# Optimization experiments

Hardware: AMD Instinct MI355X
Metric: run time of the kernel (lower is better)

The kernel has to match this reference:

```python
import jax, jax.numpy as jnp
import numpy as np

NUM_HEAD = 16
DIM_HEAD = 64
SCALE = DIM_HEAD ** -0.5


def setup_inputs() -> dict:
    key = jax.random.key(0)
    k1, k2, k3 = jax.random.split(key, 3)
    B, N, D = 4, 2048, 1024
    x = jax.random.normal(k1, (B, N, D), dtype=jnp.float32)
    w_qkv = jax.random.normal(k2, (D, 3 * NUM_HEAD * DIM_HEAD), dtype=jnp.float32) * (D ** -0.5)
    w_out = jax.random.normal(k3, (NUM_HEAD * DIM_HEAD, D), dtype=jnp.float32) * ((NUM_HEAD * DIM_HEAD) ** -0.5)
    return {"x": x, "w_qkv": w_qkv, "w_out": w_out}


def reference(x, w_qkv, w_out):
    B, N, D = x.shape
    qkv = x @ w_qkv  # [B, N, 3*H*Dh]
    q, k, v = jnp.split(qkv, 3, axis=-1)
    def heads(t):
        return t.reshape(B, N, NUM_HEAD, DIM_HEAD).transpose(0, 2, 1, 3)  # b h n d
    q, k, v = heads(q), heads(k), heads(v)
    scores = jnp.einsum('bhnd,bhmd->bhnm', q, k) * SCALE
    attn = jax.nn.softmax(scores, axis=-1)
    out = jnp.einsum('bhnm,bhmd->bhnd', attn, v)
    out = out.transpose(0, 2, 1, 3).reshape(B, N, NUM_HEAD * DIM_HEAD)
    return out @ w_out
```

## Files before the change

### kernel.cpp

```cpp
#include <hip/hip_runtime.h>
#include <hip/hip_bf16.h>
#include <stdint.h>


typedef __attribute__((ext_vector_type(8))) __bf16 bf16x8;
typedef __attribute__((ext_vector_type(4))) __bf16 bf16x4;
typedef __attribute__((ext_vector_type(4))) float f32x4;
typedef __attribute__((ext_vector_type(16))) float f32x16;
typedef __attribute__((ext_vector_type(4))) unsigned int u32x4;

#define EXPC 0.18033688011112042f
#define MC2 32.0f

static __device__ __forceinline__ void gload_lds16(const void* g, void* s) {
  __builtin_amdgcn_global_load_lds(
      (__attribute__((address_space(1))) unsigned int*)g,
      (__attribute__((address_space(3))) unsigned int*)s, 16, 0, 0);
}

__global__ void k_cvt(const float* __restrict__ src, __bf16* __restrict__ dst, int n4) {
  int i = blockIdx.x * blockDim.x + threadIdx.x;
  if (i >= n4) return;
  float4 v = reinterpret_cast<const float4*>(src)[i];
  bf16x4 o = { (__bf16)v.x, (__bf16)v.y, (__bf16)v.z, (__bf16)v.w };
  *reinterpret_cast<bf16x4*>(dst + (size_t)i * 4) = o;
}

__global__ void k_tcvt(const float* __restrict__ src, __bf16* __restrict__ dst, int W, int Hs) {
  __shared__ float tile[32][33];
  int tx = threadIdx.x, ty = threadIdx.y;
  int x = blockIdx.x * 32 + tx;
  int y0 = blockIdx.y * 32;
  for (int j = ty; j < 32; j += 8) tile[j][tx] = src[(size_t)(y0 + j) * W + x];
  __syncthreads();
  int xo = y0 + tx;
  int yo = blockIdx.x * 32;
  for (int j = ty; j < 32; j += 8) dst[(size_t)(yo + j) * Hs + xo] = (__bf16)tile[tx][j];
}

static __device__ __forceinline__ void gemm256_core8(
    const __bf16* __restrict__ A, const __bf16* __restrict__ BT, int K,
    int m0, int n0, f32x4 acc[8][4], __bf16* S) {
  const int tid = threadIdx.x;
  const int lane = tid & 63, wid = tid >> 6;
  const int fr = lane & 15, fq = lane >> 4;
  const int fr7 = fr & 7;
  const int wm = wid >> 2, wn = wid & 3;
  const int srow = tid >> 3;
  const int schunk = (tid & 7) ^ (srow & 7);
  const int NT = K >> 6;

#pragma unroll
  for (int mi = 0; mi < 8; ++mi)
#pragma unroll
    for (int nj = 0; nj < 4; ++nj) acc[mi][nj] = (f32x4){0.f, 0.f, 0.f, 0.f};

  auto stage_panel = [&](int buf, int kt, int which) {
    const __bf16* G = which ? BT : A;
    const int base0 = which ? n0 : m0;
    __bf16* L = S + buf * 32768 + which * 16384 + wid * 512;
#pragma unroll
    for (int i = 0; i < 4; ++i)
      gload_lds16(G + (size_t)(base0 + i * 64 + srow) * K + kt * 64 + schunk * 8,
                  L + i * 4096);
  };

  stage_panel(0, 0, 0); stage_panel(0, 0, 1);
  stage_panel(1, 1, 0); stage_panel(1, 1, 1);
  asm volatile("s_waitcnt vmcnt(8)" ::: "memory");
  __builtin_amdgcn_s_barrier();
  __builtin_amdgcn_sched_barrier(0);

  for (int kt = 0; kt < NT; ++kt) {
    const int c = kt & 1;
    const __bf16* Sa = S + c * 32768;
    const __bf16* Sb = Sa + 16384;
    bf16x8 af0[8], bf0[4], af1[8], bf1[4];

#pragma unroll
    for (int mi = 0; mi < 8; ++mi)
      af0[mi] = *(const bf16x8*)(Sa + (wm * 128 + mi * 16 + fr) * 64 + ((fq ^ fr7) << 3));
#pragma unroll
    for (int nj = 0; nj < 4; ++nj)
      bf0[nj] = *(const bf16x8*)(Sb + (wn * 64 + nj * 16 + fr) * 64 + ((fq ^ fr7) << 3));
    asm volatile("s_waitcnt lgkmcnt(0)" ::: "memory");
    __builtin_amdgcn_sched_barrier(0);
    __builtin_amdgcn_s_setprio(1);
#pragma unroll
    for (int mi = 0; mi < 8; ++mi)
#pragma unroll
      for (int nj = 0; nj < 2; ++nj)
        acc[mi][nj] = __builtin_amdgcn_mfma_f32_16x16x32_bf16(af0[mi], bf0[nj], acc[mi][nj], 0, 0, 0);
    __builtin_amdgcn_s_setprio(0);

#pragma unroll
    for (int mi = 0; mi < 8; ++mi)
      af1[mi] = *(const bf16x8*)(Sa + (wm * 128 + mi * 16 + fr) * 64 + (((4 + fq) ^ fr7) << 3));
#pragma unroll
    for (int nj = 0; nj < 4; ++nj)
      bf1[nj] = *(const bf16x8*)(Sb + (wn * 64 + nj * 16 + fr) * 64 + (((4 + fq) ^ fr7) << 3));
    __builtin_amdgcn_s_setprio(1);
#pragma unroll
    for (int mi = 0; mi < 8; ++mi)
#pragma unroll
      for (int nj = 2; nj < 4; ++nj)
        acc[mi][nj] = __builtin_amdgcn_mfma_f32_16x16x32_bf16(af0[mi], bf0[nj], acc[mi][nj], 0, 0, 0);
    __builtin_amdgcn_s_setprio(0);
    asm volatile("s_waitcnt lgkmcnt(0)" ::: "memory");
    __builtin_amdgcn_s_barrier();
    __builtin_amdgcn_sched_barrier(0);

    if (kt + 2 < NT) stage_panel(c, kt + 2, 0);
    __builtin_amdgcn_s_setprio(1);
#pragma unroll
    for (int mi = 0; mi < 8; ++mi)
#pragma unroll
      for (int nj = 0; nj < 2; ++nj)
        acc[mi][nj] = __builtin_amdgcn_mfma_f32_16x16x32_bf16(af1[mi], bf1[nj], acc[mi][nj], 0, 0, 0);
    __builtin_amdgcn_s_setprio(0);

    if (kt + 2 < NT) stage_panel(c, kt + 2, 1);
    __builtin_amdgcn_s_setprio(1);
#pragma unroll
    for (int mi = 0; mi < 8; ++mi)
#pragma unroll
      for (int nj = 2; nj < 4; ++nj)
        acc[mi][nj] = __builtin_amdgcn_mfma_f32_16x16x32_bf16(af1[mi], bf1[nj], acc[mi][nj], 0, 0, 0);
    __builtin_amdgcn_s_setprio(0);

    if (kt < NT - 1) {
      if (kt + 2 < NT) asm volatile("s_waitcnt vmcnt(8)" ::: "memory");
      else             asm volatile("s_waitcnt vmcnt(0)" ::: "memory");
      __builtin_amdgcn_s_barrier();
      __builtin_amdgcn_sched_barrier(0);
    }
  }
}

__global__ __launch_bounds__(512, 2) void k_gemm_qkv(
    const __bf16* __restrict__ A, const __bf16* __restrict__ BT,
    __bf16* __restrict__ qb, __bf16* __restrict__ kb, __bf16* __restrict__ vb) {
  __shared__ __align__(16) __bf16 S[2 * 32768];
  f32x4 acc[8][4];
  int m0 = blockIdx.x * 256, n0 = blockIdx.y * 256;
  gemm256_core8(A, BT, 1024, m0, n0, acc, S);
  const int lane = threadIdx.x & 63, wid = threadIdx.x >> 6;
  const int fr = lane & 15, fq = lane >> 4;
  const int wm = wid >> 2, wn = wid & 3;
  const int which = n0 >> 10;
#pragma unroll
  for (int mi = 0; mi < 8; ++mi) {
#pragma unroll
    for (int nj = 0; nj < 4; ++nj) {
      int row = m0 + wm * 128 + mi * 16 + fq * 4;
      int col = n0 + wn * 64 + nj * 16 + fr;
      int rem = col & 1023, h = rem >> 6, d = rem & 63;
      int bb = row >> 11, n = row & 2047;
      int bh = bb * 16 + h;
      if (which == 2) {
        bf16x4 pk = { (__bf16)acc[mi][nj][0], (__bf16)acc[mi][nj][1],
                      (__bf16)acc[mi][nj][2], (__bf16)acc[mi][nj][3] };
        *reinterpret_cast<bf16x4*>(vb + ((size_t)bh * 64 + d) * 2048 + n) = pk;
      } else {
        __bf16* dst = (which == 0) ? qb : kb;
#pragma unroll
        for (int j = 0; j < 4; ++j)
          dst[((size_t)bh * 2048 + (n + j)) * 64 + d] = (__bf16)acc[mi][nj][j];
      }
    }
  }
}

__global__ __launch_bounds__(512, 2) void k_gemm_out(
    const __bf16* __restrict__ A, const __bf16* __restrict__ BT, float* __restrict__ C) {
  __shared__ __align__(16) __bf16 S[2 * 32768];
  f32x4 acc[8][4];
  int m0 = blockIdx.x * 256, n0 = blockIdx.y * 256;
  gemm256_core8(A, BT, 1024, m0, n0, acc, S);
  const int lane = threadIdx.x & 63, wid = threadIdx.x >> 6;
  const int fr = lane & 15, fq = lane >> 4;
  const int wm = wid >> 2, wn = wid & 3;
#pragma unroll
  for (int mi = 0; mi < 8; ++mi)
#pragma unroll
    for (int nj = 0; nj < 4; ++nj)
#pragma unroll
      for (int j = 0; j < 4; ++j)
        C[(size_t)(m0 + wm * 128 + mi * 16 + fq * 4 + j) * 1024 + n0 + wn * 64 + nj * 16 + fr] =
            acc[mi][nj][j];
}

__global__ __launch_bounds__(256, 4) void k_attn(
    const __bf16* __restrict__ qb, const __bf16* __restrict__ kb,
    const __bf16* __restrict__ vb, __bf16* __restrict__ ao) {
  __shared__ __align__(16) __bf16 Ks[2][64 * 64];
  __shared__ __align__(16) __bf16 Vs[2][64 * 64];
  const int tid = threadIdx.x, lane = tid & 63, wid = tid >> 6;
  const int r31 = lane & 31, hi = lane >> 5;
  const int lsw = (lane & 7) ^ ((lane >> 3) & 3);
  const int bh = blockIdx.x & 63, qblk = blockIdx.x >> 6;
  const __bf16* kbase = kb + (size_t)bh * 2048 * 64;
  const __bf16* vbase = vb + (size_t)bh * 64 * 2048;

  const int nbase = qblk * 128 + wid * 32;
  const __bf16* qptr = qb + ((size_t)bh * 2048 + nbase + r31) * 64;
  bf16x8 qf[4];
#pragma unroll
  for (int dd = 0; dd < 4; ++dd)
    qf[dd] = *(const bf16x8*)(qptr + dd * 16 + hi * 8);

  f32x16 o0, o1;
#pragma unroll
  for (int r = 0; r < 16; ++r) { o0[r] = 0.f; o1[r] = 0.f; }
  float lsum = 0.f;

  auto stage = [&](int buf, int j0) {
#pragma unroll
    for (int p2 = 0; p2 < 2; ++p2) {
      int row = p2 * 32 + (tid >> 3);
      int sc = (tid & 7) ^ (row & 7) ^ ((row >> 3) & 3);
      int dst = p2 * 2048 + wid * 512;
      gload_lds16(kbase + (size_t)(j0 + row) * 64 + sc * 8, &Ks[buf][dst]);
      gload_lds16(vbase + (size_t)row * 2048 + j0 + sc * 8, &Vs[buf][dst]);
    }
  };

  stage(0, 0);
  __syncthreads();

  for (int kt = 0; kt < 32; ++kt) {
    const int cur = kt & 1;
    if (kt < 31) stage(cur ^ 1, (kt + 1) * 64);

#pragma unroll
    for (int h2 = 0; h2 < 2; ++h2) {
      const int kro = h2 * 32;

      f32x16 sa;
#pragma unroll
      for (int r = 0; r < 16; ++r) sa[r] = 0.f;
      __builtin_amdgcn_s_setprio(1);
#pragma unroll
      for (int dd = 0; dd < 4; ++dd) {
        bf16x8 kf = *(const bf16x8*)(&Ks[cur][(kro + r31) * 64 + (((dd * 2 + hi) ^ lsw) << 3)]);
        sa = __builtin_amdgcn_mfma_f32_32x32x16_bf16(kf, qf[dd], sa, 0, 0, 0);
      }
      __builtin_amdgcn_s_setprio(0);

      float rs0 = 0.f, rs1 = 0.f;
      unsigned pw[8];
#pragma unroll
      for (int r = 0; r < 8; ++r) {
        float e0 = __builtin_amdgcn_exp2f(fmaf(sa[2 * r], EXPC, -MC2));
        float e1 = __builtin_amdgcn_exp2f(fmaf(sa[2 * r + 1], EXPC, -MC2));
        rs0 += e0; rs1 += e1;
        asm("v_cvt_pk_bf16_f32 %0, %1, %2" : "=v"(pw[r]) : "v"(e0), "v"(e1));
      }
      lsum += rs0 + rs1;

      __builtin_amdgcn_s_setprio(1);
#define PVSTEP(W0, W1, W2, W3, KK) do {                                              \
        unsigned a0 = (W0), a1 = (W1), b0 = (W2), b1 = (W3);                         \
        asm("v_permlane32_swap_b32 %0, %1" : "+v"(a0), "+v"(b0));                    \
        asm("v_permlane32_swap_b32 %0, %1" : "+v"(a1), "+v"(b1));                    \
        u32x4 fw = {a0, a1, b0, b1};                                                 \
        bf16x8 pa = __builtin_bit_cast(bf16x8, fw);                                  \
        bf16x8 v0 = *(const bf16x8*)(&Vs[cur][r31 * 64 + ((((KK) * 2 + hi) ^ lsw) << 3)]); \
        bf16x8 v1 = *(const bf16x8*)(&Vs[cur][(32 + r31) * 64 + ((((KK) * 2 + hi) ^ lsw) << 3)]); \
        o0 = __builtin_amdgcn_mfma_f32_32x32x16_bf16(pa, v0, o0, 0, 0, 0);           \
        o1 = __builtin_amdgcn_mfma_f32_32x32x16_bf16(pa, v1, o1, 0, 0, 0);           \
      } while (0)
      PVSTEP(pw[0], pw[1], pw[2], pw[3], 2 * h2);
      PVSTEP(pw[4], pw[5], pw[6], pw[7], 2 * h2 + 1);
#undef PVSTEP
      __builtin_amdgcn_s_setprio(0);
    }

    __syncthreads();
  }

  lsum += __shfl_xor(lsum, 32, 64);
  float inv = 1.0f / lsum;
  const int b = bh >> 4, h = bh & 15;
  __bf16* abase = ao + ((size_t)b * 2048 + nbase) * 1024 + h * 64 + r31;
#pragma unroll
  for (int r = 0; r < 16; ++r) {
    int qrow = (r & 3) + 8 * (r >> 2) + 4 * hi;
    float ir = __shfl(inv, qrow, 64);
    abase[(size_t)qrow * 1024] = (__bf16)(o0[r] * ir);
    abase[(size_t)qrow * 1024 + 32] = (__bf16)(o1[r] * ir);
  }
}

extern "C" void kernel_launch(void* const* d_in, const int* in_sizes, int n_in,
                              void* d_out, int out_size, void* d_ws, size_t ws_size,
                              hipStream_t stream) {
  (void)in_sizes; (void)n_in; (void)out_size; (void)ws_size;
  const float* x = (const float*)d_in[0];
  const float* w_qkv = (const float*)d_in[1];
  const float* w_out = (const float*)d_in[2];
  float* out = (float*)d_out;

  char* p = (char*)d_ws;
  __bf16* xb    = (__bf16*)p; p += (size_t)8192 * 1024 * 2;
  __bf16* wqkvT = (__bf16*)p; p += (size_t)3072 * 1024 * 2;
  __bf16* woutT = (__bf16*)p; p += (size_t)1024 * 1024 * 2;
  __bf16* qb    = (__bf16*)p; p += (size_t)64 * 2048 * 64 * 2;
  __bf16* kb    = (__bf16*)p; p += (size_t)64 * 2048 * 64 * 2;
  __bf16* vb    = (__bf16*)p; p += (size_t)64 * 64 * 2048 * 2;
  __bf16* ao    = (__bf16*)p; p += (size_t)8192 * 1024 * 2;

  k_cvt<<<8192, 256, 0, stream>>>(x, xb, 2097152);
  k_tcvt<<<dim3(96, 32), dim3(32, 8), 0, stream>>>(w_qkv, wqkvT, 3072, 1024);
  k_tcvt<<<dim3(32, 32), dim3(32, 8), 0, stream>>>(w_out, woutT, 1024, 1024);
  k_gemm_qkv<<<dim3(32, 12), 512, 0, stream>>>(xb, wqkvT, qb, kb, vb);
  k_attn<<<dim3(1024), dim3(256), 0, stream>>>(qb, kb, vb, ao);
  k_gemm_out<<<dim3(32, 4), 512, 0, stream>>>(ao, woutT, out);
}
```

Baseline: 193.5 us.

## Use smaller 128x128 tiles for out-projection GEMM and MFMA-based softmax row sums

The output projection GEMM moves from a 256x256 tile with 512 threads to a simpler 128x128 tile with 256 threads and a single-buffered K=32 loop. That launches 512 blocks instead of 128, giving better occupancy across the CUs. In attention, the per-lane exp row-sum accumulation and shuffle reduction are replaced by an extra MFMA against a ones vector. The row sums then come out in the same layout as the output accumulator. Costs: the new GEMM has no double-buffering or LDS swizzle, so it may suffer bank conflicts and exposed load latency, and the extra MFMA adds matrix work while accumulating sums from bf16-rounded probabilities.

```diff
diff --git a/kernel.cpp b/kernel.cpp
--- a/kernel.cpp
+++ b/kernel.cpp
@@ -36,6 +36,43 @@
   int xo = y0 + tx;
   int yo = blockIdx.x * 32;
   for (int j = ty; j < 32; j += 8) dst[(size_t)(yo + j) * Hs + xo] = (__bf16)tile[tx][j];
+}
+
+static __device__ __forceinline__ void gemm_core(
+    const __bf16* __restrict__ A, const __bf16* __restrict__ BT, int K,
+    int m0, int n0, f32x4 acc[4][4], __bf16* As, __bf16* Bs) {
+  const int tid = threadIdx.x;
+  const int lane = tid & 63, w = tid >> 6;
+  const int fr = lane & 15, fq = lane >> 4;
+  const int srow = lane >> 2, scol = (lane & 3) * 8;
+  const int wr = (w >> 1) * 64, wc = (w & 1) * 64;
+#pragma unroll
+  for (int mi = 0; mi < 4; ++mi)
+#pragma unroll
+    for (int nj = 0; nj < 4; ++nj) acc[mi][nj] = (f32x4){0.f, 0.f, 0.f, 0.f};
+
+  for (int ko = 0; ko < K; ko += 32) {
+#pragma unroll
+    for (int i = 0; i < 2; ++i) {
+      int rb = w * 32 + i * 16;
+      gload_lds16(A + (size_t)(m0 + rb + srow) * K + ko + scol, As + rb * 32);
+      gload_lds16(BT + (size_t)(n0 + rb + srow) * K + ko + scol, Bs + rb * 32);
+    }
+    __syncthreads();
+    bf16x8 af[4], bfv[4];
+#pragma unroll
+    for (int mi = 0; mi < 4; ++mi)
+      af[mi] = *(const bf16x8*)(As + (wr + mi * 16 + fr) * 32 + fq * 8);
+#pragma unroll
+    for (int nj = 0; nj < 4; ++nj)
+      bfv[nj] = *(const bf16x8*)(Bs + (wc + nj * 16 + fr) * 32 + fq * 8);
+#pragma unroll
+    for (int mi = 0; mi < 4; ++mi)
+#pragma unroll
+      for (int nj = 0; nj < 4; ++nj)
+        acc[mi][nj] = __builtin_amdgcn_mfma_f32_16x16x32_bf16(af[mi], bfv[nj], acc[mi][nj], 0, 0, 0);
+    __syncthreads();
+  }
 }
 
 static __device__ __forceinline__ void gemm256_core8(
@@ -171,22 +208,23 @@
   }
 }
 
-__global__ __launch_bounds__(512, 2) void k_gemm_out(
+__global__ __launch_bounds__(256) void k_gemm_out(
     const __bf16* __restrict__ A, const __bf16* __restrict__ BT, float* __restrict__ C) {
-  __shared__ __align__(16) __bf16 S[2 * 32768];
-  f32x4 acc[8][4];
-  int m0 = blockIdx.x * 256, n0 = blockIdx.y * 256;
-  gemm256_core8(A, BT, 1024, m0, n0, acc, S);
-  const int lane = threadIdx.x & 63, wid = threadIdx.x >> 6;
+  __shared__ __align__(16) __bf16 As[128 * 32];
+  __shared__ __align__(16) __bf16 Bs[128 * 32];
+  f32x4 acc[4][4];
+  int m0 = blockIdx.x * 128, n0 = blockIdx.y * 128;
+  gemm_core(A, BT, 1024, m0, n0, acc, As, Bs);
+  const int lane = threadIdx.x & 63, w = threadIdx.x >> 6;
   const int fr = lane & 15, fq = lane >> 4;
-  const int wm = wid >> 2, wn = wid & 3;
-#pragma unroll
-  for (int mi = 0; mi < 8; ++mi)
+  const int wr = (w >> 1) * 64, wc = (w & 1) * 64;
+#pragma unroll
+  for (int mi = 0; mi < 4; ++mi)
 #pragma unroll
     for (int nj = 0; nj < 4; ++nj)
 #pragma unroll
       for (int j = 0; j < 4; ++j)
-        C[(size_t)(m0 + wm * 128 + mi * 16 + fq * 4 + j) * 1024 + n0 + wn * 64 + nj * 16 + fr] =
+        C[(size_t)(m0 + wr + mi * 16 + fq * 4 + j) * 1024 + n0 + wc + nj * 16 + fr] =
             acc[mi][nj][j];
 }
 
@@ -209,10 +247,12 @@
   for (int dd = 0; dd < 4; ++dd)
     qf[dd] = *(const bf16x8*)(qptr + dd * 16 + hi * 8);
 
-  f32x16 o0, o1;
-#pragma unroll
-  for (int r = 0; r < 16; ++r) { o0[r] = 0.f; o1[r] = 0.f; }
-  float lsum = 0.f;
+  const u32x4 onesw = {0x3F803F80u, 0x3F803F80u, 0x3F803F80u, 0x3F803F80u};
+  const bf16x8 onesv = __builtin_bit_cast(bf16x8, onesw);
+
+  f32x16 o0, o1, lacc;
+#pragma unroll
+  for (int r = 0; r < 16; ++r) { o0[r] = 0.f; o1[r] = 0.f; lacc[r] = 0.f; }
 
   auto stage = [&](int buf, int j0) {
 #pragma unroll
@@ -247,16 +287,13 @@
       }
       __builtin_amdgcn_s_setprio(0);
 
-      float rs0 = 0.f, rs1 = 0.f;
       unsigned pw[8];
 #pragma unroll
       for (int r = 0; r < 8; ++r) {
         float e0 = __builtin_amdgcn_exp2f(fmaf(sa[2 * r], EXPC, -MC2));
         float e1 = __builtin_amdgcn_exp2f(fmaf(sa[2 * r + 1], EXPC, -MC2));
-        rs0 += e0; rs1 += e1;
         asm("v_cvt_pk_bf16_f32 %0, %1, %2" : "=v"(pw[r]) : "v"(e0), "v"(e1));
       }
-      lsum += rs0 + rs1;
 
       __builtin_amdgcn_s_setprio(1);
 #define PVSTEP(W0, W1, W2, W3, KK) do {                                              \
@@ -269,6 +306,7 @@
         bf16x8 v1 = *(const bf16x8*)(&Vs[cur][(32 + r31) * 64 + ((((KK) * 2 + hi) ^ lsw) << 3)]); \
         o0 = __builtin_amdgcn_mfma_f32_32x32x16_bf16(pa, v0, o0, 0, 0, 0);           \
         o1 = __builtin_amdgcn_mfma_f32_32x32x16_bf16(pa, v1, o1, 0, 0, 0);           \
+        lacc = __builtin_amdgcn_mfma_f32_32x32x16_bf16(pa, onesv, lacc, 0, 0, 0);    \
       } while (0)
       PVSTEP(pw[0], pw[1], pw[2], pw[3], 2 * h2);
       PVSTEP(pw[4], pw[5], pw[6], pw[7], 2 * h2 + 1);
@@ -279,14 +317,12 @@
     __syncthreads();
   }
 
-  lsum += __shfl_xor(lsum, 32, 64);
-  float inv = 1.0f / lsum;
   const int b = bh >> 4, h = bh & 15;
   __bf16* abase = ao + ((size_t)b * 2048 + nbase) * 1024 + h * 64 + r31;
 #pragma unroll
   for (int r = 0; r < 16; ++r) {
     int qrow = (r & 3) + 8 * (r >> 2) + 4 * hi;
-    float ir = __shfl(inv, qrow, 64);
+    float ir = 1.0f / lacc[r];
     abase[(size_t)qrow * 1024] = (__bf16)(o0[r] * ir);
     abase[(size_t)qrow * 1024 + 32] = (__bf16)(o1[r] * ir);
   }
@@ -315,5 +351,5 @@
   k_tcvt<<<dim3(32, 32), dim3(32, 8), 0, stream>>>(w_out, woutT, 1024, 1024);
   k_gemm_qkv<<<dim3(32, 12), 512, 0, stream>>>(xb, wqkvT, qb, kb, vb);
   k_attn<<<dim3(1024), dim3(256), 0, stream>>>(qb, kb, vb, ao);
-  k_gemm_out<<<dim3(32, 4), 512, 0, stream>>>(ao, woutT, out);
-}
+  k_gemm_out<<<dim3(64, 8), 256, 0, stream>>>(ao, woutT, out);
+}
```

Result: no change. 193.0 us (-0.3%).
